# Optimization experiments

Hardware: AMD Instinct MI355X
Metric: run time of the kernel (lower is better)

Reference implementation:

```python
import jax, jax.numpy as jnp
import numpy as np

N, E, IN, H, HEADS, L, OUT = 4096, 262144, 64, 128, 4, 2, 2
DH = H // HEADS  # 32, per-head dim for both GAT and global MHA
BN_EPS = 1e-5
NEG_SLOPE = 0.2  # GATConv leaky_relu default


def setup_inputs() -> dict:
    key = jax.random.key(0)
    ks = iter(jax.random.split(key, 32))
    rn = lambda shape, s: jax.random.normal(next(ks), shape, jnp.float32) * s
    return {
        "x": rn((N, IN), 1.0),
        "edge_index": jax.random.randint(next(ks), (2, E), 0, N),
        "w_in": rn((H, IN), IN ** -0.5),
        "b_in": rn((H,), 0.02),
        "w_gat": rn((L, H, H), H ** -0.5),
        "att_src": rn((L, HEADS, DH), 0.1),
        "att_dst": rn((L, HEADS, DH), 0.1),
        "b_gat": rn((L, H), 0.02),
        "w_qkv": rn((L, 3 * H, H), H ** -0.5),
        "b_qkv": rn((L, 3 * H), 0.02),
        "w_o": rn((L, H, H), H ** -0.5),
        "b_o": rn((L, H), 0.02),
        "bn_gamma": 1.0 + rn((L, 3, H), 0.05),
        "bn_beta": rn((L, 3, H), 0.05),
        "w1": rn((L, 2 * H, H), H ** -0.5),
        "b1": rn((L, 2 * H), 0.02),
        "w2": rn((L, H, 2 * H), (2 * H) ** -0.5),
        "b2": rn((L, H), 0.02),
        "w_out": rn((OUT, H), H ** -0.5),
        "b_out": rn((OUT,), 0.02),
    }


def _bn(h, g, b):
    # eval-mode BatchNorm1d with running_mean=0, running_var=1
    return h * (g / jnp.sqrt(1.0 + BN_EPS)) + b


def _gat(x, src, dst, w, a_src, a_dst, bias):
    # GATConv(hidden, hidden//heads, heads=HEADS, add_self_loops=False), concat=True
    xp = (x @ w.T).reshape(N, HEADS, DH)                  # [N, HEADS, DH]
    al_s = jnp.einsum('nhd,hd->nh', xp, a_src)            # [N, HEADS]
    al_d = jnp.einsum('nhd,hd->nh', xp, a_dst)
    logit = al_s[src] + al_d[dst]                         # [E, HEADS]
    logit = jnp.where(logit >= 0, logit, NEG_SLOPE * logit)
    m = jax.ops.segment_max(logit, dst, num_segments=N)   # scatter-softmax over dst
    m = jnp.where(jnp.isfinite(m), m, 0.0)
    e = jnp.exp(logit - m[dst])
    denom = jax.ops.segment_sum(e, dst, num_segments=N)
    alpha = e / (denom[dst] + 1e-16)
    out = jax.ops.segment_sum(alpha[:, :, None] * xp[src], dst, num_segments=N)
    return out.reshape(N, H) + bias


def _mha(x, wqkv, bqkv, wo, bo):
    # torch.nn.MultiheadAttention self-attention over all N nodes (one graph)
    qkv = x @ wqkv.T + bqkv
    q, k, v = jnp.split(qkv, 3, axis=-1)
    q = q.reshape(N, HEADS, DH)
    k = k.reshape(N, HEADS, DH)
    v = v.reshape(N, HEADS, DH)
    scores = jnp.einsum('nhd,mhd->hnm', q, k) / jnp.sqrt(jnp.float32(DH))
    attn = jax.nn.softmax(scores, axis=-1)
    out = jnp.einsum('hnm,mhd->nhd', attn, v).reshape(N, H)
    return out @ wo.T + bo


def reference(x, edge_index, w_in, b_in, w_gat, att_src, att_dst, b_gat,
              w_qkv, b_qkv, w_o, b_o, bn_gamma, bn_beta,
              w1, b1, w2, b2, w_out, b_out):
    src, dst = edge_index[0], edge_index[1]
    h = jax.nn.relu(x @ w_in.T + b_in)
    for l in range(L):
        # GPSConv: local GAT branch (dropout inactive in eval)
        h_loc = _gat(h, src, dst, w_gat[l], att_src[l], att_dst[l], b_gat[l]) + h
        h_loc = _bn(h_loc, bn_gamma[l, 0], bn_beta[l, 0])
        # GPSConv: global attention branch
        h_att = _mha(h, w_qkv[l], b_qkv[l], w_o[l], b_o[l]) + h
        h_att = _bn(h_att, bn_gamma[l, 1], bn_beta[l, 1])
        out = h_loc + h_att
        mlp = jax.nn.relu(out @ w1[l].T + b1[l]) @ w2[l].T + b2[l]
        out = _bn(out + mlp, bn_gamma[l, 2], bn_beta[l, 2])
        # GPSRiskModel residual + relu (dropout inactive in eval)
        h = jax.nn.relu(out + h)
    return h @ w_out.T + b_out
```

## Files before the change

### kernel.cpp

```cpp
#include <hip/hip_runtime.h>

#define NN 4096
#define EE 262144
#define INF_ 64
#define HH 128
#define HEADS 4
#define DH 32
#define LL 2
#define NH (NN * HH)
#define KSPLIT 8
#define L2E 1.4426950408889634f

typedef unsigned short u16;
typedef unsigned int u32;
using bf16x8 = __attribute__((ext_vector_type(8))) short;
using f32x4 = __attribute__((ext_vector_type(4))) float;

__device__ __forceinline__ float bf2f(u16 v) { return __uint_as_float(((u32)v) << 16); }
__device__ __forceinline__ u16 f2bf(float f) {
    u32 u = __float_as_uint(f);
    u32 r = (u + 0x7fffu + ((u >> 16) & 1u)) >> 16;
    return (u16)r;
}
__device__ __forceinline__ u32 encf(float f) {
    u32 b = __float_as_uint(f);
    return (b & 0x80000000u) ? ~b : (b | 0x80000000u);
}
__device__ __forceinline__ float decf(u32 u) {
    u32 b = (u & 0x80000000u) ? (u & 0x7fffffffu) : ~u;
    return __uint_as_float(b);
}

__global__ __launch_bounds__(256) void k_detect(const u16* __restrict__ x, int* __restrict__ flag) {
    __shared__ int cs[256];
    int t = threadIdx.x;
    u16 v = x[2 * t];
    int e = (v >> 7) & 0xFF;
    cs[t] = (e >= 100 && e <= 140) ? 1 : 0;
    __syncthreads();
    for (int s = 128; s > 0; s >>= 1) {
        if (t < s) cs[t] += cs[t + s];
        __syncthreads();
    }
    if (t == 0) *flag = (cs[0] >= 128) ? 1 : 0;
}

#define MAXSEG 16
struct SegF { const void* src[MAXSEG]; int dst[MAXSEG]; int n[MAXSEG]; int cnt; };
__global__ void k_cvtf(SegF S, float* __restrict__ W, const int* __restrict__ flag) {
    int seg = blockIdx.y;
    if (seg >= S.cnt) return;
    int n = S.n[seg];
    float* d = W + S.dst[seg];
    const void* s = S.src[seg];
    int f = *flag;
    for (int i = blockIdx.x * 256 + threadIdx.x; i < n; i += gridDim.x * 256)
        d[i] = f ? bf2f(((const u16*)s)[i]) : ((const float*)s)[i];
}
struct SegB { const void* src[8]; u16* dst[8]; int n[8]; int cnt; };
__global__ void k_cvtb(SegB S, const int* __restrict__ flag) {
    int seg = blockIdx.y;
    if (seg >= S.cnt) return;
    int n = S.n[seg];
    u16* d = S.dst[seg];
    const void* s = S.src[seg];
    int f = *flag;
    for (int i = blockIdx.x * 256 + threadIdx.x; i < n; i += gridDim.x * 256)
        d[i] = f ? ((const u16*)s)[i] : f2bf(((const float*)s)[i]);
}

__global__ void k_split(const void* __restrict__ src, u16* __restrict__ hi, u16* __restrict__ lo,
                        int n, const int* __restrict__ flag) {
    int i = blockIdx.x * blockDim.x + threadIdx.x;
    if (i >= n) return;
    float v = *flag ? bf2f(((const u16*)src)[i]) : ((const float*)src)[i];
    u16 h = f2bf(v);
    hi[i] = h;
    lo[i] = f2bf(v - bf2f(h));
}

__global__ void k_zero(int* cnt, u32* gmax) {
    int t = blockIdx.x * blockDim.x + threadIdx.x;
    if (t < NN) cnt[t] = 0;
    if (t < 16) gmax[t] = 0;
}
__global__ void k_hist(const int* __restrict__ dst, int* __restrict__ cnt) {
    int e = blockIdx.x * blockDim.x + threadIdx.x;
    if (e < EE) atomicAdd(&cnt[dst[e]], 1);
}
__global__ __launch_bounds__(256) void k_scan(const int* __restrict__ cnt, int* __restrict__ rowstart,
                                              int* __restrict__ cursor) {
    __shared__ int part[256];
    int t = threadIdx.x;
    int loc[16];
    int s = 0;
#pragma unroll
    for (int i = 0; i < 16; ++i) { loc[i] = s; s += cnt[t * 16 + i]; }
    part[t] = s;
    __syncthreads();
    for (int off = 1; off < 256; off <<= 1) {
        int v = part[t];
        int a = (t >= off) ? part[t - off] : 0;
        __syncthreads();
        part[t] = v + a;
        __syncthreads();
    }
    int base = (t == 0) ? 0 : part[t - 1];
#pragma unroll
    for (int i = 0; i < 16; ++i) {
        rowstart[t * 16 + i] = base + loc[i];
        cursor[t * 16 + i] = base + loc[i];
    }
}
__global__ void k_scatter(const int* __restrict__ src, const int* __restrict__ dst,
                          int* __restrict__ cursor, int* __restrict__ esrc) {
    int e = blockIdx.x * blockDim.x + threadIdx.x;
    if (e < EE) {
        int d = dst[e];
        int p = atomicAdd(&cursor[d], 1);
        esrc[p] = src[e];
    }
}

__global__ __launch_bounds__(128) void k_mgemm(const u16* __restrict__ Ahi, const u16* __restrict__ Alo,
                                               const u16* __restrict__ Wb, const float* __restrict__ bias,
                                               float* __restrict__ outf, u16* __restrict__ outb16,
                                               u16* __restrict__ outhi, u16* __restrict__ outlo,
                                               int K, int J, int relu) {
    int wave = threadIdx.x >> 6, lane = threadIdx.x & 63;
    int grp = lane >> 4, lcol = lane & 15;
    int m0 = blockIdx.x * 32 + wave * 16;
    int j0 = blockIdx.y * 64;
    f32x4 acc[4];
#pragma unroll
    for (int s = 0; s < 4; ++s) acc[s] = (f32x4){0.f, 0.f, 0.f, 0.f};
    const u16* ah = Ahi + (size_t)(m0 + lcol) * K + grp * 8;
    const u16* al = Alo + (size_t)(m0 + lcol) * K + grp * 8;
    const u16* wb = Wb + (size_t)(j0 + lcol) * K + grp * 8;
    for (int k = 0; k < K; k += 32) {
        bf16x8 va = *(const bf16x8*)(ah + k);
        bf16x8 vl = *(const bf16x8*)(al + k);
#pragma unroll
        for (int s = 0; s < 4; ++s) {
            bf16x8 vw = *(const bf16x8*)(wb + (size_t)s * 16 * K + k);
            acc[s] = __builtin_amdgcn_mfma_f32_16x16x32_bf16(va, vw, acc[s], 0, 0, 0);
            acc[s] = __builtin_amdgcn_mfma_f32_16x16x32_bf16(vl, vw, acc[s], 0, 0, 0);
        }
    }
#pragma unroll
    for (int s = 0; s < 4; ++s) {
        int col = j0 + s * 16 + lcol;
        float bs = bias ? bias[col] : 0.f;
#pragma unroll
        for (int r = 0; r < 4; ++r) {
            float v = acc[s][r] + bs;
            if (relu) v = fmaxf(v, 0.f);
            size_t idx = (size_t)(m0 + grp * 4 + r) * J + col;
            if (outf) outf[idx] = v;
            if (outb16) outb16[idx] = f2bf(v);
            if (outhi) {
                u16 hv = f2bf(v);
                outhi[idx] = hv;
                outlo[idx] = f2bf(v - bf2f(hv));
            }
        }
    }
}

__global__ __launch_bounds__(128) void k_gemm_gq(const u16* __restrict__ Ahi, const u16* __restrict__ Alo,
                                                 const u16* __restrict__ wgat, const u16* __restrict__ wqkv,
                                                 const float* __restrict__ bqkv,
                                                 float* __restrict__ xpf, u16* __restrict__ xpb,
                                                 u16* __restrict__ qkvb) {
    int wave = threadIdx.x >> 6, lane = threadIdx.x & 63;
    int grp = lane >> 4, lcol = lane & 15;
    int m0 = blockIdx.x * 32 + wave * 16;
    int jb = blockIdx.y;
    int j0 = jb * 64;
    const u16* Wb = (jb < 2) ? (wgat + (size_t)j0 * HH) : (wqkv + (size_t)(j0 - 128) * HH);
    f32x4 acc[4];
#pragma unroll
    for (int s = 0; s < 4; ++s) acc[s] = (f32x4){0.f, 0.f, 0.f, 0.f};
    const u16* ah = Ahi + (size_t)(m0 + lcol) * HH + grp * 8;
    const u16* al = Alo + (size_t)(m0 + lcol) * HH + grp * 8;
    const u16* wb = Wb + (size_t)lcol * HH + grp * 8;
    for (int k = 0; k < HH; k += 32) {
        bf16x8 va = *(const bf16x8*)(ah + k);
        bf16x8 vl = *(const bf16x8*)(al + k);
#pragma unroll
        for (int s = 0; s < 4; ++s) {
            bf16x8 vw = *(const bf16x8*)(wb + (size_t)s * 16 * HH + k);
            acc[s] = __builtin_amdgcn_mfma_f32_16x16x32_bf16(va, vw, acc[s], 0, 0, 0);
            acc[s] = __builtin_amdgcn_mfma_f32_16x16x32_bf16(vl, vw, acc[s], 0, 0, 0);
        }
    }
    if (jb < 2) {
#pragma unroll
        for (int s = 0; s < 4; ++s) {
            int col = j0 + s * 16 + lcol;
#pragma unroll
            for (int r = 0; r < 4; ++r) {
                float v = acc[s][r];
                size_t idx = (size_t)(m0 + grp * 4 + r) * HH + col;
                xpf[idx] = v;
                xpb[idx] = f2bf(v);
            }
        }
    } else {
#pragma unroll
        for (int s = 0; s < 4; ++s) {
            int colq = j0 - 128 + s * 16 + lcol;
            float bs = bqkv[colq];
#pragma unroll
            for (int r = 0; r < 4; ++r)
                qkvb[(size_t)(m0 + grp * 4 + r) * 384 + colq] = f2bf(acc[s][r] + bs);
        }
    }
}

__global__ __launch_bounds__(128) void k_gemm_wo(const u16* __restrict__ Ahi, const u16* __restrict__ Alo,
                                                 const u16* __restrict__ Wb, const float* __restrict__ bias,
                                                 const float* __restrict__ gatb, const float* __restrict__ hbuf,
                                                 const float* __restrict__ bgat, const float* __restrict__ gam,
                                                 const float* __restrict__ bet,
                                                 float* __restrict__ outb, u16* __restrict__ ohi,
                                                 u16* __restrict__ olo) {
    int wave = threadIdx.x >> 6, lane = threadIdx.x & 63;
    int grp = lane >> 4, lcol = lane & 15;
    int m0 = blockIdx.x * 32 + wave * 16;
    int j0 = blockIdx.y * 64;
    f32x4 acc[4];
#pragma unroll
    for (int s = 0; s < 4; ++s) acc[s] = (f32x4){0.f, 0.f, 0.f, 0.f};
    const u16* ah = Ahi + (size_t)(m0 + lcol) * HH + grp * 8;
    const u16* al = Alo + (size_t)(m0 + lcol) * HH + grp * 8;
    const u16* wb = Wb + (size_t)(j0 + lcol) * HH + grp * 8;
    for (int k = 0; k < HH; k += 32) {
        bf16x8 va = *(const bf16x8*)(ah + k);
        bf16x8 vl = *(const bf16x8*)(al + k);
#pragma unroll
        for (int s = 0; s < 4; ++s) {
            bf16x8 vw = *(const bf16x8*)(wb + (size_t)s * 16 * HH + k);
            acc[s] = __builtin_amdgcn_mfma_f32_16x16x32_bf16(va, vw, acc[s], 0, 0, 0);
            acc[s] = __builtin_amdgcn_mfma_f32_16x16x32_bf16(vl, vw, acc[s], 0, 0, 0);
        }
    }
    float rs = rsqrtf(1.00001f);
#pragma unroll
    for (int s = 0; s < 4; ++s) {
        int col = j0 + s * 16 + lcol;
        float bs = bias[col];
        float g0 = gam[col] * rs, b0 = bet[col];
        float g1 = gam[HH + col] * rs, b1 = bet[HH + col];
        float bg = bgat[col];
#pragma unroll
        for (int r = 0; r < 4; ++r) {
            size_t idx = (size_t)(m0 + grp * 4 + r) * HH + col;
            float proj = acc[s][r] + bs;
            float hv = hbuf[idx];
            float hl = g0 * (gatb[idx] + bg + hv) + b0;
            float ha = g1 * (proj + hv) + b1;
            float v = hl + ha;
            outb[idx] = v;
            u16 hb = f2bf(v);
            ohi[idx] = hb;
            olo[idx] = f2bf(v - bf2f(hb));
        }
    }
}

__global__ __launch_bounds__(128) void k_gemm_w2(const u16* __restrict__ Ahi, const u16* __restrict__ Alo,
                                                 const u16* __restrict__ Wb, const float* __restrict__ bias,
                                                 const float* __restrict__ outb, const float* __restrict__ gam2,
                                                 const float* __restrict__ bet2,
                                                 float* __restrict__ hbuf, u16* __restrict__ hhi,
                                                 u16* __restrict__ hlo) {
    int wave = threadIdx.x >> 6, lane = threadIdx.x & 63;
    int grp = lane >> 4, lcol = lane & 15;
    int m0 = blockIdx.x * 32 + wave * 16;
    int j0 = blockIdx.y * 64;
    const int K = 2 * HH;
    f32x4 acc[4];
#pragma unroll
    for (int s = 0; s < 4; ++s) acc[s] = (f32x4){0.f, 0.f, 0.f, 0.f};
    const u16* ah = Ahi + (size_t)(m0 + lcol) * K + grp * 8;
    const u16* al = Alo + (size_t)(m0 + lcol) * K + grp * 8;
    const u16* wb = Wb + (size_t)(j0 + lcol) * K + grp * 8;
    for (int k = 0; k < K; k += 32) {
        bf16x8 va = *(const bf16x8*)(ah + k);
        bf16x8 vl = *(const bf16x8*)(al + k);
#pragma unroll
        for (int s = 0; s < 4; ++s) {
            bf16x8 vw = *(const bf16x8*)(wb + (size_t)s * 16 * K + k);
            acc[s] = __builtin_amdgcn_mfma_f32_16x16x32_bf16(va, vw, acc[s], 0, 0, 0);
            acc[s] = __builtin_amdgcn_mfma_f32_16x16x32_bf16(vl, vw, acc[s], 0, 0, 0);
        }
    }
    float rs = rsqrtf(1.00001f);
#pragma unroll
    for (int s = 0; s < 4; ++s) {
        int col = j0 + s * 16 + lcol;
        float bs = bias[col];
        float g2 = gam2[col] * rs, b2 = bet2[col];
#pragma unroll
        for (int r = 0; r < 4; ++r) {
            size_t idx = (size_t)(m0 + grp * 4 + r) * HH + col;
            float mlpo = acc[s][r] + bs;
            float o2 = g2 * (outb[idx] + mlpo) + b2;
            float v = fmaxf(o2 + hbuf[idx], 0.f);
            hbuf[idx] = v;
            u16 hb = f2bf(v);
            hhi[idx] = hb;
            hlo[idx] = f2bf(v - bf2f(hb));
        }
    }
}

__global__ __launch_bounds__(256) void k_attlog(const float* __restrict__ xp, const float* __restrict__ asrc,
                                                const float* __restrict__ adst, float* __restrict__ als,
                                                float* __restrict__ ald, u32* __restrict__ gmax) {
    int t = blockIdx.x * 256 + threadIdx.x;
    int n = t >> 2, hh = t & 3;
    const float* xr = xp + (size_t)n * HH + hh * DH;
    float s1 = 0.f, s2 = 0.f;
#pragma unroll
    for (int d = 0; d < DH; ++d) {
        float v = xr[d];
        s1 += v * asrc[hh * DH + d];
        s2 += v * adst[hh * DH + d];
    }
    als[t] = s1;
    ald[t] = s2;
    __shared__ float red[256];
    int lt = threadIdx.x;
    red[lt] = s1;
    __syncthreads();
    for (int off = 128; off >= 4; off >>= 1) {
        if (lt < off) red[lt] = fmaxf(red[lt], red[lt + off]);
        __syncthreads();
    }
    if (lt < 4) atomicMax(&gmax[lt], encf(red[lt]));
    __syncthreads();
    red[lt] = s2;
    __syncthreads();
    for (int off = 128; off >= 4; off >>= 1) {
        if (lt < off) red[lt] = fmaxf(red[lt], red[lt + off]);
        __syncthreads();
    }
    if (lt < 4) atomicMax(&gmax[4 + lt], encf(red[lt]));
}

#define GCHUNK 256
__global__ __launch_bounds__(128) void k_gat_node(const int* __restrict__ esrc, const int* __restrict__ rowstart,
                                                  const int* __restrict__ cnt, const float* __restrict__ als,
                                                  const float* __restrict__ ald, const u16* __restrict__ xpb,
                                                  float* __restrict__ gatout, const u32* __restrict__ gmax) {
    int n = blockIdx.x, t = threadIdx.x;
    int base = rowstart[n], c = cnt[n];
    float4 adv = ((const float4*)ald)[n];
    float ad[4] = {adv.x, adv.y, adv.z, adv.w};
    float M2[4];
#pragma unroll
    for (int h = 0; h < 4; ++h) {
        float bound = decf(gmax[h]) + decf(gmax[4 + h]);
        float M = bound >= 0.f ? bound : 0.2f * bound;
        M2[h] = M * L2E;
    }
    __shared__ float red[512];
    __shared__ float elds[GCHUNK * 4];
    __shared__ int slds[GCHUNK];
    float dsum[4] = {0.f, 0.f, 0.f, 0.f};
    float acc = 0.f;
    int ht = t >> 5;
    for (int ch = 0; ch < c; ch += GCHUNK) {
        int cn = min(GCHUNK, c - ch);
        __syncthreads();
        for (int i = t; i < cn; i += 128) {
            int s = esrc[base + ch + i];
            slds[i] = s;
            float4 as = ((const float4*)als)[s];
            float lg, e;
            lg = as.x + ad[0]; lg = lg >= 0.f ? lg : 0.2f * lg; e = __builtin_exp2f(lg * L2E - M2[0]); elds[i * 4 + 0] = e; dsum[0] += e;
            lg = as.y + ad[1]; lg = lg >= 0.f ? lg : 0.2f * lg; e = __builtin_exp2f(lg * L2E - M2[1]); elds[i * 4 + 1] = e; dsum[1] += e;
            lg = as.z + ad[2]; lg = lg >= 0.f ? lg : 0.2f * lg; e = __builtin_exp2f(lg * L2E - M2[2]); elds[i * 4 + 2] = e; dsum[2] += e;
            lg = as.w + ad[3]; lg = lg >= 0.f ? lg : 0.2f * lg; e = __builtin_exp2f(lg * L2E - M2[3]); elds[i * 4 + 3] = e; dsum[3] += e;
        }
        __syncthreads();
        int i = 0;
        for (; i + 2 <= cn; i += 2) {
            int s0 = slds[i], s1 = slds[i + 1];
            float e0 = elds[i * 4 + ht], e1 = elds[(i + 1) * 4 + ht];
            float x0 = bf2f(xpb[(size_t)s0 * HH + t]);
            float x1 = bf2f(xpb[(size_t)s1 * HH + t]);
            acc += e0 * x0 + e1 * x1;
        }
        if (i < cn) acc += elds[i * 4 + ht] * bf2f(xpb[(size_t)slds[i] * HH + t]);
    }
    __syncthreads();
#pragma unroll
    for (int h = 0; h < 4; ++h) red[h * 128 + t] = dsum[h];
    __syncthreads();
    for (int s2 = 64; s2 > 0; s2 >>= 1) {
        if (t < s2) {
#pragma unroll
            for (int h = 0; h < 4; ++h)
                red[h * 128 + t] += red[h * 128 + t + s2];
        }
        __syncthreads();
    }
    float inv = 1.f / (red[ht * 128] + 1e-16f);
    gatout[(size_t)n * HH + t] = acc * inv;
}

__global__ __launch_bounds__(256) void k_mha_split(const u16* __restrict__ qkvb,
                                                   float* __restrict__ PM, float* __restrict__ PL,
                                                   float* __restrict__ PO) {
    const float C1 = 0.17677669529663687f * L2E;
    int head = blockIdx.x & 3;
    int qt = (blockIdx.x >> 2) & 63;
    int ks = blockIdx.x >> 8;
    int tid = threadIdx.x;
    int wave = tid >> 6, lane = tid & 63;
    int grp = lane >> 4, lcol = lane & 15;

    __shared__ __align__(16) u16 Klds[64][40];
    __shared__ __align__(16) u32 Vlds[32][36];
    __shared__ __align__(16) u16 Plds[4][16][66];

    int qrow0 = qt * 64 + wave * 16;
    bf16x8 aQ = *(const bf16x8*)(qkvb + (size_t)(qrow0 + lcol) * 384 + head * 32 + grp * 8);

    f32x4 oc0 = {0.f, 0.f, 0.f, 0.f}, oc1 = {0.f, 0.f, 0.f, 0.f};
    float msh = -INFINITY;
    float lrow[4] = {0.f, 0.f, 0.f, 0.f};

    int isK = (tid < 128);
    int st = tid & 127;
    int skey = st >> 1, shalf = (st & 1) * 16;
    int vj = st & 31, dgrp = st >> 5;
    int vkey0 = 32 * (vj & 1) + (vj >> 1);
    const u16* kptr = qkvb + 128 + head * 32 + shalf;
    const u16* vptr = qkvb + 256 + head * 32 + dgrp * 8;

    int kt0 = ks * (NN / KSPLIT);
    bf16x8 r0, r1;
    if (isK) {
        r0 = *(const bf16x8*)(kptr + (size_t)(kt0 + skey) * 384);
        r1 = *(const bf16x8*)(kptr + (size_t)(kt0 + skey) * 384 + 8);
    } else {
        r0 = *(const bf16x8*)(vptr + (size_t)(kt0 + vkey0) * 384);
        r1 = *(const bf16x8*)(vptr + (size_t)(kt0 + vkey0 + 16) * 384);
    }

    const int NT = (NN / KSPLIT) / 64;
    for (int t = 0; t < NT; ++t) {
        if (isK) {
            *(bf16x8*)(&Klds[skey][shalf]) = r0;
            *(bf16x8*)(&Klds[skey][shalf + 8]) = r1;
        } else {
#pragma unroll
            for (int j = 0; j < 8; ++j)
                Vlds[dgrp * 8 + j][vj] = (u32)(u16)r0[j] | ((u32)(u16)r1[j] << 16);
        }
        __syncthreads();
        if (t + 1 < NT) {
            int kn = kt0 + (t + 1) * 64;
            if (isK) {
                r0 = *(const bf16x8*)(kptr + (size_t)(kn + skey) * 384);
                r1 = *(const bf16x8*)(kptr + (size_t)(kn + skey) * 384 + 8);
            } else {
                r0 = *(const bf16x8*)(vptr + (size_t)(kn + vkey0) * 384);
                r1 = *(const bf16x8*)(vptr + (size_t)(kn + vkey0 + 16) * 384);
            }
        }
        f32x4 sc[4];
        f32x4 zero = {0.f, 0.f, 0.f, 0.f};
#pragma unroll
        for (int s = 0; s < 4; ++s) {
            bf16x8 bK = *(const bf16x8*)(&Klds[s * 16 + lcol][grp * 8]);
            sc[s] = __builtin_amdgcn_mfma_f32_16x16x32_bf16(aQ, bK, zero, 0, 0, 0);
        }
        float tv[4][4];
        float mymax = -INFINITY;
#pragma unroll
        for (int s = 0; s < 4; ++s)
#pragma unroll
            for (int r = 0; r < 4; ++r) {
                float x = sc[s][r] * C1;
                tv[s][r] = x;
                mymax = fmaxf(mymax, x);
            }
        mymax = fmaxf(mymax, __shfl_xor(mymax, 1));
        mymax = fmaxf(mymax, __shfl_xor(mymax, 2));
        mymax = fmaxf(mymax, __shfl_xor(mymax, 4));
        mymax = fmaxf(mymax, __shfl_xor(mymax, 8));
        float mnew = fmaxf(msh, mymax);
        float cc = __builtin_exp2f(msh - mnew);
        msh = mnew;
#pragma unroll
        for (int r = 0; r < 4; ++r) {
            float p0 = __builtin_exp2f(tv[0][r] - mnew);
            float p1 = __builtin_exp2f(tv[1][r] - mnew);
            float p2 = __builtin_exp2f(tv[2][r] - mnew);
            float p3 = __builtin_exp2f(tv[3][r] - mnew);
            lrow[r] = lrow[r] * cc + ((p0 + p1) + (p2 + p3));
            u32 lo01 = (__float_as_uint(p0) >> 16) | (__float_as_uint(p1) & 0xffff0000u);
            u32 lo23 = (__float_as_uint(p2) >> 16) | (__float_as_uint(p3) & 0xffff0000u);
            *(uint2*)(&Plds[wave][grp * 4 + r][4 * lcol]) = make_uint2(lo01, lo23);
        }
        oc0 *= cc;
        oc1 *= cc;
#pragma unroll
        for (int c2 = 0; c2 < 2; ++c2) {
            bf16x8 aP = *(const bf16x8*)(&Plds[wave][lcol][c2 * 32 + grp * 8]);
            bf16x8 bV0 = *(const bf16x8*)(&Vlds[lcol][c2 * 16 + grp * 4]);
            bf16x8 bV1 = *(const bf16x8*)(&Vlds[16 + lcol][c2 * 16 + grp * 4]);
            oc0 = __builtin_amdgcn_mfma_f32_16x16x32_bf16(aP, bV0, oc0, 0, 0, 0);
            oc1 = __builtin_amdgcn_mfma_f32_16x16x32_bf16(aP, bV1, oc1, 0, 0, 0);
        }
        __syncthreads();
    }
#pragma unroll
    for (int r = 0; r < 4; ++r) {
        lrow[r] += __shfl_xor(lrow[r], 1);
        lrow[r] += __shfl_xor(lrow[r], 2);
        lrow[r] += __shfl_xor(lrow[r], 4);
        lrow[r] += __shfl_xor(lrow[r], 8);
    }
#pragma unroll
    for (int r = 0; r < 4; ++r) {
        int row = qrow0 + grp * 4 + r;
        size_t base = ((size_t)row * HEADS + head) * KSPLIT + ks;
        PO[base * 32 + lcol] = oc0[r];
        PO[base * 32 + 16 + lcol] = oc1[r];
        if (lcol == 0) {
            PM[base] = msh;
            PL[base] = lrow[r];
        }
    }
}

__global__ void k_mha_comb(const float* __restrict__ PM, const float* __restrict__ PL,
                           const float* __restrict__ PO, u16* __restrict__ atthi,
                           u16* __restrict__ attlo) {
    int t = blockIdx.x * 256 + threadIdx.x;
    if (t >= NN * HH) return;
    int row = t >> 7, col = t & 127;
    int head = col >> 5, dim = col & 31;
    size_t b0 = ((size_t)row * HEADS + head) * KSPLIT;
    float m = -INFINITY;
#pragma unroll
    for (int k = 0; k < KSPLIT; ++k) m = fmaxf(m, PM[b0 + k]);
    float l = 0.f, o = 0.f;
#pragma unroll
    for (int k = 0; k < KSPLIT; ++k) {
        float w = __builtin_exp2f(PM[b0 + k] - m);
        l += PL[b0 + k] * w;
        o += PO[(b0 + k) * 32 + dim] * w;
    }
    float v = o / l;
    u16 h = f2bf(v);
    atthi[t] = h;
    attlo[t] = f2bf(v - bf2f(h));
}

__global__ __launch_bounds__(64) void k_out(const float* __restrict__ h, const float* __restrict__ w,
                                            const float* __restrict__ b, void* __restrict__ yout,
                                            const int* __restrict__ flag) {
    int n = blockIdx.x, l = threadIdx.x;
    float a0 = 0.f, a1 = 0.f;
    for (int k = l; k < HH; k += 64) {
        float hv = h[(size_t)n * HH + k];
        a0 += hv * w[k];
        a1 += hv * w[HH + k];
    }
#pragma unroll
    for (int off = 32; off > 0; off >>= 1) {
        a0 += __shfl_xor(a0, off);
        a1 += __shfl_xor(a1, off);
    }
    if (l == 0) {
        float o0 = a0 + b[0], o1 = a1 + b[1];
        if (*flag) {
            u16* y = (u16*)yout;
            y[n * 2 + 0] = f2bf(o0);
            y[n * 2 + 1] = f2bf(o1);
        } else {
            float* y = (float*)yout;
            y[n * 2 + 0] = o0;
            y[n * 2 + 1] = o1;
        }
    }
}

extern "C" void kernel_launch(void* const* d_in, const int* in_sizes, int n_in,
                              void* d_out, int out_size, void* d_ws, size_t ws_size,
                              hipStream_t stream) {
    float* W = (float*)d_ws;
    size_t o = 0;
    auto take = [&](size_t n) { size_t r = o; o += n; return r; };
    size_t pb_in = take(HH);
    size_t pattS = take(LL * HEADS * DH);
    size_t pattD = take(LL * HEADS * DH);
    size_t pb_gat = take(LL * HH);
    size_t pb_qkv = take(LL * 3 * HH);
    size_t pb_o  = take(LL * HH);
    size_t pbn_g = take(LL * 3 * HH);
    size_t pbn_b = take(LL * 3 * HH);
    size_t pb1   = take(LL * 2 * HH);
    size_t pb2   = take(LL * HH);
    size_t pw_out = take(2 * HH);
    size_t pb_out = take(2);
    auto takeb = [&](size_t nu16) { size_t r = o; o += (nu16 + 1) / 2; return r; };
    size_t bw_in  = takeb(HH * INF_);
    size_t bw_gat = takeb(LL * HH * HH);
    size_t bw_qkv = takeb(LL * 3 * HH * HH);
    size_t bw_o   = takeb(LL * HH * HH);
    size_t bw1    = takeb(LL * 2 * HH * HH);
    size_t bw2    = takeb(LL * HH * 2 * HH);
    o = (o + 127) & ~(size_t)127;
    size_t ohbuf = take(NH);
    size_t ogat  = take(NH);
    size_t otmp  = take(NH);
    size_t oals  = take(NN * HEADS);
    size_t oald  = take(NN * HEADS);
    size_t opm   = take(NN * HEADS * KSPLIT);
    size_t opl   = take(NN * HEADS * KSPLIT);
    size_t opo   = take((size_t)NN * HEADS * KSPLIT * 32);
    size_t oqkvb = takeb(NN * 384);
    size_t oxpb  = takeb(NH);
    size_t oxhi  = takeb(NN * INF_);
    size_t oxlo  = takeb(NN * INF_);
    size_t ohhi  = takeb(NH);
    size_t ohlo  = takeb(NH);
    size_t oahi  = takeb(NH);
    size_t oalo  = takeb(NH);
    size_t oohi  = takeb(NH);
    size_t oolo  = takeb(NH);
    size_t omhi  = takeb(NN * 2 * HH);
    size_t omlo  = takeb(NN * 2 * HH);
    int* ibase    = (int*)(W + o);
    int* iflag    = ibase;
    int* cnt      = ibase + 64;
    int* rowstart = cnt + NN;
    int* cursor   = rowstart + NN;
    int* esrc     = cursor + NN;
    u32* gmax     = (u32*)(esrc + EE);

    float* hbuf = W + ohbuf;
    float* gatb = W + ogat;
    float* tmp  = W + otmp;
    float* als  = W + oals;
    float* ald  = W + oald;
    float* pmb  = W + opm;
    float* plb  = W + opl;
    float* pob  = W + opo;
    u16* qkvb = (u16*)(W + oqkvb);
    u16* xpb  = (u16*)(W + oxpb);
    u16* xhi = (u16*)(W + oxhi), *xlo = (u16*)(W + oxlo);
    u16* hhi = (u16*)(W + ohhi), *hlo = (u16*)(W + ohlo);
    u16* ahi = (u16*)(W + oahi), *alo = (u16*)(W + oalo);
    u16* ohi = (u16*)(W + oohi), *olo = (u16*)(W + oolo);
    u16* mhi = (u16*)(W + omhi), *mlo = (u16*)(W + omlo);

    const int* src = (const int*)d_in[1];
    const int* dst = (const int*)d_in[1] + EE;

    k_detect<<<1, 256, 0, stream>>>((const u16*)d_in[0], iflag);

    SegF SF = {};
    int nf = 0;
    auto addf = [&](int idx, size_t off, int n) { SF.src[nf] = d_in[idx]; SF.dst[nf] = (int)off; SF.n[nf] = n; ++nf; };
    addf(3, pb_in, HH);
    addf(5, pattS, LL * HEADS * DH);
    addf(6, pattD, LL * HEADS * DH);
    addf(7, pb_gat, LL * HH);
    addf(9, pb_qkv, LL * 3 * HH);
    addf(11, pb_o, LL * HH);
    addf(12, pbn_g, LL * 3 * HH);
    addf(13, pbn_b, LL * 3 * HH);
    addf(15, pb1, LL * 2 * HH);
    addf(17, pb2, LL * HH);
    addf(18, pw_out, 2 * HH);
    addf(19, pb_out, 2);
    SF.cnt = nf;
    k_cvtf<<<dim3(8, nf), 256, 0, stream>>>(SF, W, iflag);

    SegB SB = {};
    int nb = 0;
    auto addb = [&](int idx, size_t off, int n) { SB.src[nb] = d_in[idx]; SB.dst[nb] = (u16*)(W + off); SB.n[nb] = n; ++nb; };
    addb(2, bw_in, HH * INF_);
    addb(4, bw_gat, LL * HH * HH);
    addb(8, bw_qkv, LL * 3 * HH * HH);
    addb(10, bw_o, LL * HH * HH);
    addb(14, bw1, LL * 2 * HH * HH);
    addb(16, bw2, LL * HH * 2 * HH);
    SB.cnt = nb;
    k_cvtb<<<dim3(128, nb), 256, 0, stream>>>(SB, iflag);

    k_split<<<(NN * INF_) / 256, 256, 0, stream>>>(d_in[0], xhi, xlo, NN * INF_, iflag);

    k_zero<<<16, 256, 0, stream>>>(cnt, gmax);
    k_hist<<<EE / 256, 256, 0, stream>>>(dst, cnt);
    k_scan<<<1, 256, 0, stream>>>(cnt, rowstart, cursor);
    k_scatter<<<EE / 256, 256, 0, stream>>>(src, dst, cursor, esrc);

    k_mgemm<<<dim3(NN / 32, HH / 64), 128, 0, stream>>>(xhi, xlo, (u16*)(W + bw_in), W + pb_in,
                                                        hbuf, nullptr, hhi, hlo, INF_, HH, 1);

    for (int l = 0; l < LL; ++l) {
        k_gemm_gq<<<dim3(NN / 32, 8), 128, 0, stream>>>(hhi, hlo,
                                                        (u16*)(W + bw_gat) + (size_t)l * HH * HH,
                                                        (u16*)(W + bw_qkv) + (size_t)l * 3 * HH * HH,
                                                        W + pb_qkv + l * 3 * HH, tmp, xpb, qkvb);
        k_attlog<<<(NN * HEADS) / 256, 256, 0, stream>>>(tmp, W + pattS + l * HEADS * DH,
                                                         W + pattD + l * HEADS * DH, als, ald,
                                                         gmax + l * 8);
        k_gat_node<<<NN, 128, 0, stream>>>(esrc, rowstart, cnt, als, ald, xpb, gatb, gmax + l * 8);
        k_mha_split<<<(NN / 64) * HEADS * KSPLIT, 256, 0, stream>>>(qkvb, pmb, plb, pob);
        k_mha_comb<<<(NN * HH) / 256, 256, 0, stream>>>(pmb, plb, pob, ahi, alo);
        k_gemm_wo<<<dim3(NN / 32, HH / 64), 128, 0, stream>>>(ahi, alo,
                                                              (u16*)(W + bw_o) + (size_t)l * HH * HH,
                                                              W + pb_o + l * HH, gatb, hbuf,
                                                              W + pb_gat + l * HH, W + pbn_g + l * 3 * HH,
                                                              W + pbn_b + l * 3 * HH, tmp, ohi, olo);
        k_mgemm<<<dim3(NN / 32, 256 / 64), 128, 0, stream>>>(ohi, olo,
                                                             (u16*)(W + bw1) + (size_t)l * 2 * HH * HH,
                                                             W + pb1 + l * 2 * HH, nullptr, nullptr,
                                                             mhi, mlo, HH, 2 * HH, 1);
        k_gemm_w2<<<dim3(NN / 32, HH / 64), 128, 0, stream>>>(mhi, mlo,
                                                              (u16*)(W + bw2) + (size_t)l * HH * 2 * HH,
                                                              W + pb2 + l * HH, tmp,
                                                              W + pbn_g + l * 3 * HH + 2 * HH,
                                                              W + pbn_b + l * 3 * HH + 2 * HH,
                                                              hbuf, hhi, hlo);
    }
    k_out<<<NN, 64, 0, stream>>>(hbuf, W + pw_out, W + pb_out, d_out, iflag);
}
```

Baseline: 335.0 us.

## Fuse attention logits into GAT GEMM, merge setup kernels, bf16 MHA partials

```diff
diff --git a/kernel.cpp b/kernel.cpp
--- a/kernel.cpp
+++ b/kernel.cpp
@@ -31,9 +31,12 @@
     return __uint_as_float(b);
 }
 
-__global__ __launch_bounds__(256) void k_detect(const u16* __restrict__ x, int* __restrict__ flag) {
+__global__ __launch_bounds__(256) void k_detect(const u16* __restrict__ x, int* __restrict__ flag,
+                                                int* __restrict__ cnt, u32* __restrict__ gmax) {
+    int t = threadIdx.x;
+    for (int i = t; i < NN; i += 256) cnt[i] = 0;
+    if (t < 16) gmax[t] = 0;
     __shared__ int cs[256];
-    int t = threadIdx.x;
     u16 v = x[2 * t];
     int e = (v >> 7) & 0xFF;
     cs[t] = (e >= 100 && e <= 140) ? 1 : 0;
@@ -57,33 +60,27 @@
     for (int i = blockIdx.x * 256 + threadIdx.x; i < n; i += gridDim.x * 256)
         d[i] = f ? bf2f(((const u16*)s)[i]) : ((const float*)s)[i];
 }
-struct SegB { const void* src[8]; u16* dst[8]; int n[8]; int cnt; };
+struct SegB { const void* src[8]; u16* dst[8]; u16* dst2[8]; int n[8]; int cnt; };
 __global__ void k_cvtb(SegB S, const int* __restrict__ flag) {
     int seg = blockIdx.y;
     if (seg >= S.cnt) return;
     int n = S.n[seg];
     u16* d = S.dst[seg];
+    u16* d2 = S.dst2[seg];
     const void* s = S.src[seg];
     int f = *flag;
-    for (int i = blockIdx.x * 256 + threadIdx.x; i < n; i += gridDim.x * 256)
-        d[i] = f ? ((const u16*)s)[i] : f2bf(((const float*)s)[i]);
-}
-
-__global__ void k_split(const void* __restrict__ src, u16* __restrict__ hi, u16* __restrict__ lo,
-                        int n, const int* __restrict__ flag) {
-    int i = blockIdx.x * blockDim.x + threadIdx.x;
-    if (i >= n) return;
-    float v = *flag ? bf2f(((const u16*)src)[i]) : ((const float*)src)[i];
-    u16 h = f2bf(v);
-    hi[i] = h;
-    lo[i] = f2bf(v - bf2f(h));
-}
-
-__global__ void k_zero(int* cnt, u32* gmax) {
-    int t = blockIdx.x * blockDim.x + threadIdx.x;
-    if (t < NN) cnt[t] = 0;
-    if (t < 16) gmax[t] = 0;
-}
+    for (int i = blockIdx.x * 256 + threadIdx.x; i < n; i += gridDim.x * 256) {
+        if (d2) {
+            float v = f ? bf2f(((const u16*)s)[i]) : ((const float*)s)[i];
+            u16 h = f2bf(v);
+            d[i] = h;
+            d2[i] = f2bf(v - bf2f(h));
+        } else {
+            d[i] = f ? ((const u16*)s)[i] : f2bf(((const float*)s)[i]);
+        }
+    }
+}
+
 __global__ void k_hist(const int* __restrict__ dst, int* __restrict__ cnt) {
     int e = blockIdx.x * blockDim.x + threadIdx.x;
     if (e < EE) atomicAdd(&cnt[dst[e]], 1);
@@ -170,8 +167,10 @@
 __global__ __launch_bounds__(128) void k_gemm_gq(const u16* __restrict__ Ahi, const u16* __restrict__ Alo,
                                                  const u16* __restrict__ wgat, const u16* __restrict__ wqkv,
                                                  const float* __restrict__ bqkv,
-                                                 float* __restrict__ xpf, u16* __restrict__ xpb,
-                                                 u16* __restrict__ qkvb) {
+                                                 const float* __restrict__ attS, const float* __restrict__ attD,
+                                                 u16* __restrict__ xpb, u16* __restrict__ qkvb,
+                                                 float* __restrict__ als, float* __restrict__ ald,
+                                                 u32* __restrict__ gmax) {
     int wave = threadIdx.x >> 6, lane = threadIdx.x & 63;
     int grp = lane >> 4, lcol = lane & 15;
     int m0 = blockIdx.x * 32 + wave * 16;
@@ -199,12 +198,55 @@
         for (int s = 0; s < 4; ++s) {
             int col = j0 + s * 16 + lcol;
 #pragma unroll
-            for (int r = 0; r < 4; ++r) {
-                float v = acc[s][r];
-                size_t idx = (size_t)(m0 + grp * 4 + r) * HH + col;
-                xpf[idx] = v;
-                xpb[idx] = f2bf(v);
+            for (int r = 0; r < 4; ++r)
+                xpb[(size_t)(m0 + grp * 4 + r) * HH + col] = f2bf(acc[s][r]);
+        }
+        float as_[4], ad_[4];
+#pragma unroll
+        for (int s = 0; s < 4; ++s) {
+            int h = jb * 2 + (s >> 1);
+            int d = (s & 1) * 16 + lcol;
+            as_[s] = attS[h * DH + d];
+            ad_[s] = attD[h * DH + d];
+        }
+        float m_s0 = -INFINITY, m_s1 = -INFINITY, m_d0 = -INFINITY, m_d1 = -INFINITY;
+#pragma unroll
+        for (int r = 0; r < 4; ++r) {
+            float s01 = acc[0][r] * as_[0] + acc[1][r] * as_[1];
+            float d01 = acc[0][r] * ad_[0] + acc[1][r] * ad_[1];
+            float s23 = acc[2][r] * as_[2] + acc[3][r] * as_[3];
+            float d23 = acc[2][r] * ad_[2] + acc[3][r] * ad_[3];
+#pragma unroll
+            for (int off = 1; off <= 8; off <<= 1) {
+                s01 += __shfl_xor(s01, off);
+                d01 += __shfl_xor(d01, off);
+                s23 += __shfl_xor(s23, off);
+                d23 += __shfl_xor(d23, off);
             }
+            if (lcol == 0) {
+                int n = m0 + grp * 4 + r;
+                als[n * 4 + jb * 2] = s01;
+                als[n * 4 + jb * 2 + 1] = s23;
+                ald[n * 4 + jb * 2] = d01;
+                ald[n * 4 + jb * 2 + 1] = d23;
+            }
+            m_s0 = fmaxf(m_s0, s01);
+            m_s1 = fmaxf(m_s1, s23);
+            m_d0 = fmaxf(m_d0, d01);
+            m_d1 = fmaxf(m_d1, d23);
+        }
+#pragma unroll
+        for (int off = 16; off <= 32; off <<= 1) {
+            m_s0 = fmaxf(m_s0, __shfl_xor(m_s0, off));
+            m_s1 = fmaxf(m_s1, __shfl_xor(m_s1, off));
+            m_d0 = fmaxf(m_d0, __shfl_xor(m_d0, off));
+            m_d1 = fmaxf(m_d1, __shfl_xor(m_d1, off));
+        }
+        if (lane == 0) {
+            atomicMax(&gmax[jb * 2], encf(m_s0));
+            atomicMax(&gmax[jb * 2 + 1], encf(m_s1));
+            atomicMax(&gmax[4 + jb * 2], encf(m_d0));
+            atomicMax(&gmax[4 + jb * 2 + 1], encf(m_d1));
         }
     } else {
 #pragma unroll
@@ -314,40 +356,6 @@
             hlo[idx] = f2bf(v - bf2f(hb));
         }
     }
-}
-
-__global__ __launch_bounds__(256) void k_attlog(const float* __restrict__ xp, const float* __restrict__ asrc,
-                                                const float* __restrict__ adst, float* __restrict__ als,
-                                                float* __restrict__ ald, u32* __restrict__ gmax) {
-    int t = blockIdx.x * 256 + threadIdx.x;
-    int n = t >> 2, hh = t & 3;
-    const float* xr = xp + (size_t)n * HH + hh * DH;
-    float s1 = 0.f, s2 = 0.f;
-#pragma unroll
-    for (int d = 0; d < DH; ++d) {
-        float v = xr[d];
-        s1 += v * asrc[hh * DH + d];
-        s2 += v * adst[hh * DH + d];
-    }
-    als[t] = s1;
-    ald[t] = s2;
-    __shared__ float red[256];
-    int lt = threadIdx.x;
-    red[lt] = s1;
-    __syncthreads();
-    for (int off = 128; off >= 4; off >>= 1) {
-        if (lt < off) red[lt] = fmaxf(red[lt], red[lt + off]);
-        __syncthreads();
-    }
-    if (lt < 4) atomicMax(&gmax[lt], encf(red[lt]));
-    __syncthreads();
-    red[lt] = s2;
-    __syncthreads();
-    for (int off = 128; off >= 4; off >>= 1) {
-        if (lt < off) red[lt] = fmaxf(red[lt], red[lt + off]);
-        __syncthreads();
-    }
-    if (lt < 4) atomicMax(&gmax[4 + lt], encf(red[lt]));
 }
 
 #define GCHUNK 256
@@ -414,7 +422,7 @@
 
 __global__ __launch_bounds__(256) void k_mha_split(const u16* __restrict__ qkvb,
                                                    float* __restrict__ PM, float* __restrict__ PL,
-                                                   float* __restrict__ PO) {
+                                                   u16* __restrict__ PO) {
     const float C1 = 0.17677669529663687f * L2E;
     int head = blockIdx.x & 3;
     int qt = (blockIdx.x >> 2) & 63;
@@ -430,9 +438,11 @@
     int qrow0 = qt * 64 + wave * 16;
     bf16x8 aQ = *(const bf16x8*)(qkvb + (size_t)(qrow0 + lcol) * 384 + head * 32 + grp * 8);
 
-    f32x4 oc0 = {0.f, 0.f, 0.f, 0.f}, oc1 = {0.f, 0.f, 0.f, 0.f};
+    short onev = (lcol == 0) ? (short)0x3F80 : (short)0;
+    bf16x8 bOne = {onev, onev, onev, onev, onev, onev, onev, onev};
+
+    f32x4 oc0 = {0.f, 0.f, 0.f, 0.f}, oc1 = {0.f, 0.f, 0.f, 0.f}, ol = {0.f, 0.f, 0.f, 0.f};
     float msh = -INFINITY;
-    float lrow[4] = {0.f, 0.f, 0.f, 0.f};
 
     int isK = (tid < 128);
     int st = tid & 127;
@@ -480,36 +490,31 @@
             bf16x8 bK = *(const bf16x8*)(&Klds[s * 16 + lcol][grp * 8]);
             sc[s] = __builtin_amdgcn_mfma_f32_16x16x32_bf16(aQ, bK, zero, 0, 0, 0);
         }
-        float tv[4][4];
-        float mymax = -INFINITY;
+        float mymax = sc[0][0];
 #pragma unroll
         for (int s = 0; s < 4; ++s)
 #pragma unroll
-            for (int r = 0; r < 4; ++r) {
-                float x = sc[s][r] * C1;
-                tv[s][r] = x;
-                mymax = fmaxf(mymax, x);
-            }
+            for (int r = 0; r < 4; ++r) mymax = fmaxf(mymax, sc[s][r]);
         mymax = fmaxf(mymax, __shfl_xor(mymax, 1));
         mymax = fmaxf(mymax, __shfl_xor(mymax, 2));
         mymax = fmaxf(mymax, __shfl_xor(mymax, 4));
         mymax = fmaxf(mymax, __shfl_xor(mymax, 8));
-        float mnew = fmaxf(msh, mymax);
+        float mnew = fmaxf(msh, mymax * C1);
         float cc = __builtin_exp2f(msh - mnew);
         msh = mnew;
 #pragma unroll
         for (int r = 0; r < 4; ++r) {
-            float p0 = __builtin_exp2f(tv[0][r] - mnew);
-            float p1 = __builtin_exp2f(tv[1][r] - mnew);
-            float p2 = __builtin_exp2f(tv[2][r] - mnew);
-            float p3 = __builtin_exp2f(tv[3][r] - mnew);
-            lrow[r] = lrow[r] * cc + ((p0 + p1) + (p2 + p3));
-            u32 lo01 = (__float_as_uint(p0) >> 16) | (__float_as_uint(p1) & 0xffff0000u);
-            u32 lo23 = (__float_as_uint(p2) >> 16) | (__float_as_uint(p3) & 0xffff0000u);
-            *(uint2*)(&Plds[wave][grp * 4 + r][4 * lcol]) = make_uint2(lo01, lo23);
+            float p0 = __builtin_exp2f(__builtin_fmaf(sc[0][r], C1, -mnew));
+            float p1 = __builtin_exp2f(__builtin_fmaf(sc[1][r], C1, -mnew));
+            float p2 = __builtin_exp2f(__builtin_fmaf(sc[2][r], C1, -mnew));
+            float p3 = __builtin_exp2f(__builtin_fmaf(sc[3][r], C1, -mnew));
+            u32 pk01 = __builtin_amdgcn_perm(__float_as_uint(p1), __float_as_uint(p0), 0x07060302u);
+            u32 pk23 = __builtin_amdgcn_perm(__float_as_uint(p3), __float_as_uint(p2), 0x07060302u);
+            *(uint2*)(&Plds[wave][grp * 4 + r][4 * lcol]) = make_uint2(pk01, pk23);
         }
         oc0 *= cc;
         oc1 *= cc;
+        ol *= cc;
 #pragma unroll
         for (int c2 = 0; c2 < 2; ++c2) {
             bf16x8 aP = *(const bf16x8*)(&Plds[wave][lcol][c2 * 32 + grp * 8]);
@@ -517,31 +522,25 @@
             bf16x8 bV1 = *(const bf16x8*)(&Vlds[16 + lcol][c2 * 16 + grp * 4]);
             oc0 = __builtin_amdgcn_mfma_f32_16x16x32_bf16(aP, bV0, oc0, 0, 0, 0);
             oc1 = __builtin_amdgcn_mfma_f32_16x16x32_bf16(aP, bV1, oc1, 0, 0, 0);
+            ol = __builtin_amdgcn_mfma_f32_16x16x32_bf16(aP, bOne, ol, 0, 0, 0);
         }
         __syncthreads();
-    }
-#pragma unroll
-    for (int r = 0; r < 4; ++r) {
-        lrow[r] += __shfl_xor(lrow[r], 1);
-        lrow[r] += __shfl_xor(lrow[r], 2);
-        lrow[r] += __shfl_xor(lrow[r], 4);
-        lrow[r] += __shfl_xor(lrow[r], 8);
     }
 #pragma unroll
     for (int r = 0; r < 4; ++r) {
         int row = qrow0 + grp * 4 + r;
         size_t base = ((size_t)row * HEADS + head) * KSPLIT + ks;
-        PO[base * 32 + lcol] = oc0[r];
-        PO[base * 32 + 16 + lcol] = oc1[r];
+        PO[base * 32 + lcol] = f2bf(oc0[r]);
+        PO[base * 32 + 16 + lcol] = f2bf(oc1[r]);
         if (lcol == 0) {
             PM[base] = msh;
-            PL[base] = lrow[r];
+            PL[base] = ol[r];
         }
     }
 }
 
 __global__ void k_mha_comb(const float* __restrict__ PM, const float* __restrict__ PL,
-                           const float* __restrict__ PO, u16* __restrict__ atthi,
+                           const u16* __restrict__ PO, u16* __restrict__ atthi,
                            u16* __restrict__ attlo) {
     int t = blockIdx.x * 256 + threadIdx.x;
     if (t >= NN * HH) return;
@@ -556,7 +555,7 @@
     for (int k = 0; k < KSPLIT; ++k) {
         float w = __builtin_exp2f(PM[b0 + k] - m);
         l += PL[b0 + k] * w;
-        o += PO[(b0 + k) * 32 + dim] * w;
+        o += bf2f(PO[(b0 + k) * 32 + dim]) * w;
     }
     float v = o / l;
     u16 h = f2bf(v);
@@ -626,7 +625,7 @@
     size_t oald  = take(NN * HEADS);
     size_t opm   = take(NN * HEADS * KSPLIT);
     size_t opl   = take(NN * HEADS * KSPLIT);
-    size_t opo   = take((size_t)NN * HEADS * KSPLIT * 32);
+    size_t opo   = takeb((size_t)NN * HEADS * KSPLIT * 32);
     size_t oqkvb = takeb(NN * 384);
     size_t oxpb  = takeb(NH);
     size_t oxhi  = takeb(NN * INF_);
@@ -654,7 +653,7 @@
     float* ald  = W + oald;
     float* pmb  = W + opm;
     float* plb  = W + opl;
-    float* pob  = W + opo;
+    u16* pob  = (u16*)(W + opo);
     u16* qkvb = (u16*)(W + oqkvb);
     u16* xpb  = (u16*)(W + oxpb);
     u16* xhi = (u16*)(W + oxhi), *xlo = (u16*)(W + oxlo);
@@ -666,7 +665,7 @@
     const int* src = (const int*)d_in[1];
     const int* dst = (const int*)d_in[1] + EE;
 
-    k_detect<<<1, 256, 0, stream>>>((const u16*)d_in[0], iflag);
+    k_detect<<<1, 256, 0, stream>>>((const u16*)d_in[0], iflag, cnt, gmax);
 
     SegF SF = {};
     int nf = 0;
@@ -688,19 +687,19 @@
 
     SegB SB = {};
     int nb = 0;
-    auto addb = [&](int idx, size_t off, int n) { SB.src[nb] = d_in[idx]; SB.dst[nb] = (u16*)(W + off); SB.n[nb] = n; ++nb; };
-    addb(2, bw_in, HH * INF_);
-    addb(4, bw_gat, LL * HH * HH);
-    addb(8, bw_qkv, LL * 3 * HH * HH);
-    addb(10, bw_o, LL * HH * HH);
-    addb(14, bw1, LL * 2 * HH * HH);
-    addb(16, bw2, LL * HH * 2 * HH);
+    auto addb = [&](int idx, size_t off, int n, u16* d2) {
+        SB.src[nb] = d_in[idx]; SB.dst[nb] = (u16*)(W + off); SB.dst2[nb] = d2; SB.n[nb] = n; ++nb;
+    };
+    addb(2, bw_in, HH * INF_, nullptr);
+    addb(4, bw_gat, LL * HH * HH, nullptr);
+    addb(8, bw_qkv, LL * 3 * HH * HH, nullptr);
+    addb(10, bw_o, LL * HH * HH, nullptr);
+    addb(14, bw1, LL * 2 * HH * HH, nullptr);
+    addb(16, bw2, LL * HH * 2 * HH, nullptr);
+    SB.src[nb] = d_in[0]; SB.dst[nb] = xhi; SB.dst2[nb] = xlo; SB.n[nb] = NN * INF_; ++nb;
     SB.cnt = nb;
     k_cvtb<<<dim3(128, nb), 256, 0, stream>>>(SB, iflag);
 
-    k_split<<<(NN * INF_) / 256, 256, 0, stream>>>(d_in[0], xhi, xlo, NN * INF_, iflag);
-
-    k_zero<<<16, 256, 0, stream>>>(cnt, gmax);
     k_hist<<<EE / 256, 256, 0, stream>>>(dst, cnt);
     k_scan<<<1, 256, 0, stream>>>(cnt, rowstart, cursor);
     k_scatter<<<EE / 256, 256, 0, stream>>>(src, dst, cursor, esrc);
@@ -712,10 +711,10 @@
         k_gemm_gq<<<dim3(NN / 32, 8), 128, 0, stream>>>(hhi, hlo,
                                                         (u16*)(W + bw_gat) + (size_t)l * HH * HH,
                                                         (u16*)(W + bw_qkv) + (size_t)l * 3 * HH * HH,
-                                                        W + pb_qkv + l * 3 * HH, tmp, xpb, qkvb);
-        k_attlog<<<(NN * HEADS) / 256, 256, 0, stream>>>(tmp, W + pattS + l * HEADS * DH,
-                                                         W + pattD + l * HEADS * DH, als, ald,
-                                                         gmax + l * 8);
+                                                        W + pb_qkv + l * 3 * HH,
+                                                        W + pattS + l * HEADS * DH,
+                                                        W + pattD + l * HEADS * DH,
+                                                        xpb, qkvb, als, ald, gmax + l * 8);
         k_gat_node<<<NN, 128, 0, stream>>>(esrc, rowstart, cnt, als, ald, xpb, gatb, gmax + l * 8);
         k_mha_split<<<(NN / 64) * HEADS * KSPLIT, 256, 0, stream>>>(qkvb, pmb, plb, pob);
         k_mha_comb<<<(NN * HH) / 256, 256, 0, stream>>>(pmb, plb, pob, ahi, alo);
```

Measured after the change: 360.7 us. 7.7% more time.
